# Performance work log

Measured on AMD Instinct MI355X. Metric: run time of the kernel, lower is better.

## Reference

```python
import jax, jax.numpy as jnp
import numpy as np

H = 8        # num_heads
HKV = 4      # kv_heads
WINDOW = 12  # sliding-window size (Chebyshev distance on the 2D grid)
BASE = 10000.0


def _rope_tables(N, head_dim, base=BASE):
    """2D axial RoPE for a square grid: first half of head_dim -> H pos, second -> W pos."""
    side = int(round(N ** 0.5))
    assert side * side == N
    dq = head_dim // 4
    inv = 1.0 / (base ** (np.arange(dq, dtype=np.float32) / dq))
    gh, gw = np.meshgrid(np.arange(side, dtype=np.float32), np.arange(side, dtype=np.float32), indexing='ij')
    th = np.outer(gh.ravel(), inv)   # [N, dq]
    tw = np.outer(gw.ravel(), inv)   # [N, dq]
    theta = np.concatenate([th, tw], axis=1)        # [N, head_dim//2]
    theta = np.concatenate([theta, theta], axis=1)  # [N, head_dim]
    return jnp.asarray(np.cos(theta)), jnp.asarray(np.sin(theta))


def _window_mask(N, window):
    """Additive mask: -inf where Chebyshev distance on the sqrt(N) x sqrt(N) grid > window."""
    side = int(round(N ** 0.5))
    idx = np.arange(side)
    gh, gw = np.meshgrid(idx, idx, indexing='ij')
    coords = np.stack([gh.ravel(), gw.ravel()], axis=1)            # [N, 2]
    dist = np.abs(coords[:, None, :] - coords[None, :, :]).max(-1)  # [N, N]
    return jnp.asarray(np.where(dist > window, -np.inf, 0.0).astype(np.float32))


def _rotate_half(x):
    x1, x2 = jnp.split(x, 2, axis=-1)
    return jnp.concatenate([-x2, x1], axis=-1)


def _apply_rope(x, cos, sin):
    # x: [B,H,N,d]; cos/sin: [N,d] broadcast over batch/heads
    return x * cos + _rotate_half(x) * sin


def _l2norm(x, eps=1e-12):
    return x / jnp.sqrt(jnp.sum(x * x, axis=-1, keepdims=True) + eps)


def setup_inputs() -> dict:
    key = jax.random.key(0)
    ks = jax.random.split(key, 7)
    B, N, C = 4, 2304, 512
    x = jax.random.normal(ks[0], (B, N, C), dtype=jnp.float32)
    Wq = jax.random.normal(ks[1], (C, 2 * C), dtype=jnp.float32) * 0.02
    Wk = jax.random.normal(ks[2], (C, 2 * C * HKV // H), dtype=jnp.float32) * 0.02
    Wv1 = jax.random.normal(ks[3], (C, C * HKV // H), dtype=jnp.float32) * 0.02
    Wv2 = jax.random.normal(ks[4], (C, C * HKV // H), dtype=jnp.float32) * 0.02
    lambda_p = jnp.full((H, 1, 1), -2.0, dtype=jnp.float32)
    Wp = jax.random.normal(ks[5], (C, C), dtype=jnp.float32) * 0.02
    bp = jnp.zeros((C,), dtype=jnp.float32)
    return {"x": x, "Wq": Wq, "Wk": Wk, "Wv1": Wv1, "Wv2": Wv2,
            "lambda_p": lambda_p, "Wp": Wp, "bp": bp}


def reference(x, Wq, Wk, Wv1, Wv2, lambda_p, Wp, bp):
    B, N, C = x.shape
    d = C // H
    scale = d ** -0.5
    cos, sin = _rope_tables(N, d)
    mask = _window_mask(N, WINDOW)  # [N,N] additive

    def to_heads(t, h):  # [B,N,h*d] -> [B,h,N,d]
        return t.reshape(B, N, h, -1).transpose(0, 2, 1, 3)

    q = x @ Wq                                  # [B,N,2C]
    q1, q2 = jnp.split(q, 2, axis=-1)
    q1, q2 = to_heads(q1, H), to_heads(q2, H)   # [B,H,N,d]
    k = x @ Wk                                  # [B,N,2*C*HKV/H]
    k1, k2 = jnp.split(k, 2, axis=-1)
    k1, k2 = to_heads(k1, HKV), to_heads(k2, HKV)  # [B,HKV,N,d]
    v1 = to_heads(x @ Wv1, HKV)
    v2 = to_heads(x @ Wv2, HKV)

    # QK-norm (L2) then RoPE
    q1, q2, k1, k2 = (_l2norm(t) for t in (q1, q2, k1, k2))
    q1 = _apply_rope(q1, cos, sin)
    q2 = _apply_rope(q2, cos, sin)
    k1 = _apply_rope(k1, cos, sin)
    k2 = _apply_rope(k2, cos, sin)

    # GQA: repeat KV heads to match query heads
    rep = H // HKV
    k1, k2 = jnp.repeat(k1, rep, axis=1), jnp.repeat(k2, rep, axis=1)
    v1, v2 = jnp.repeat(v1, rep, axis=1), jnp.repeat(v2, rep, axis=1)

    attn1 = jax.nn.softmax(jnp.einsum('bhnd,bhmd->bhnm', q1, k1) * scale + mask, axis=-1)
    attn2 = jax.nn.softmax(jnp.einsum('bhnd,bhmd->bhnm', q2, k2) * scale + mask, axis=-1)
    lam = jax.nn.sigmoid(lambda_p)[None]  # [1,H,1,1]
    out = jnp.einsum('bhnm,bhmd->bhnd', attn1, v1) - lam * jnp.einsum('bhnm,bhmd->bhnd', attn2, v2)
    out = out.transpose(0, 2, 1, 3).reshape(B, N, C)
    return out @ Wp + bp
```

## Files before the change

### kernel.cpp

```cpp
#include <hip/hip_runtime.h>
#include <stdint.h>

typedef unsigned short u16;
typedef __attribute__((ext_vector_type(8))) short bf16x8;
typedef __attribute__((ext_vector_type(4))) float f32x4;

#define LOG2E 1.4426950408889634f

__device__ __forceinline__ float bf2f(u16 u) {
    union { uint32_t i; float f; } v; v.i = ((uint32_t)u) << 16; return v.f;
}
__device__ __forceinline__ u16 f2bf(float f) {
    union { float f; uint32_t i; } v; v.f = f;
    uint32_t i = v.i;
    return (u16)((i + 0x7FFF + ((i >> 16) & 1)) >> 16);
}
__device__ __forceinline__ uint32_t cvt_pk_bf16(float a, float b) {
    uint32_t r;
    asm("v_cvt_pk_bf16_f32 %0, %1, %2" : "=v"(r) : "v"(a), "v"(b));
    return r;
}
__device__ __forceinline__ int imin(int a, int b) { return a < b ? a : b; }
__device__ __forceinline__ int imax(int a, int b) { return a > b ? a : b; }

__device__ __forceinline__ void gl_lds16(const void* g, void* l) {
    __builtin_amdgcn_global_load_lds(
        (const __attribute__((address_space(1))) uint32_t*)g,
        (__attribute__((address_space(3))) uint32_t*)l, 16, 0, 0);
}

__device__ __forceinline__ float exp2_poly(float t) {
    const float c1 = 0.6931471805599453f;
    const float c2 = 0.2402265069591007f;
    const float c3 = 0.05550410866482158f;
    float p = fmaf(c3, t, c2);
    p = fmaf(p, t, c1);
    return fmaf(p, t, 1.0f);
}

union U8 { bf16x8 v; uint32_t u[4]; };

__global__ void k_prep(const float* __restrict__ x,
                       const float* __restrict__ Wq, const float* __restrict__ Wk,
                       const float* __restrict__ Wv1, const float* __restrict__ Wv2,
                       const float* __restrict__ Wp,
                       float* __restrict__ tab, u16* __restrict__ xb,
                       u16* __restrict__ WCT, u16* __restrict__ WPT) {
    __shared__ u16 tile[64][65];
    int bid = blockIdx.x;
    if (bid < 288) {
        int t = bid * 256 + threadIdx.x;
        if (t >= 2304 * 32) return;
        int n = t >> 5, j = t & 31;
        int gh = n / 48, gw = n % 48;
        float f = (float)(j & 15);
        float coord = (j < 16) ? (float)gh : (float)gw;
        float inv = exp2f(-f * (13.287712379549449f / 16.0f));
        float th = coord * inv;
        tab[t * 2 + 0] = cosf(th);
        tab[t * 2 + 1] = sinf(th);
    } else if (bid < 4896) {
        int t = (bid - 288) * 256 + threadIdx.x;
        if (t >= 9216 * 512 / 4) return;
        float4 v = ((const float4*)x)[t];
        ushort4 o;
        o.x = f2bf(v.x); o.y = f2bf(v.y); o.z = f2bf(v.z); o.w = f2bf(v.w);
        ((ushort4*)xb)[t] = o;
    } else {
        int jb = bid - 4896;
        int n0 = (jb % 40) * 64;
        int k0 = (jb / 40) * 64;
        int c = threadIdx.x & 63;
        int rr = threadIdx.x >> 6;
        const float* src; int stride; int roff; u16* dst; int nb;
        if (n0 < 1024)      { src = Wq;  stride = 1024; roff = 0;    dst = WCT; nb = n0; }
        else if (n0 < 1536) { src = Wk;  stride = 512;  roff = 1024; dst = WCT; nb = n0; }
        else if (n0 < 1792) { src = Wv1; stride = 256;  roff = 1536; dst = WCT; nb = n0; }
        else if (n0 < 2048) { src = Wv2; stride = 256;  roff = 1792; dst = WCT; nb = n0; }
        else                { src = Wp;  stride = 512;  roff = 2048; dst = WPT; nb = n0 - 2048; }
        int scol = n0 + c - roff;
#pragma unroll
        for (int i = 0; i < 16; ++i) {
            int k = rr * 16 + i;
            tile[c][k] = f2bf(src[(size_t)(k0 + k) * stride + scol]);
        }
        __syncthreads();
        int kk = threadIdx.x & 63;
        int c4 = threadIdx.x >> 6;
#pragma unroll
        for (int i = 0; i < 16; ++i) {
            int nl = c4 * 16 + i;
            dst[(size_t)(nb + nl) * 512 + k0 + kk] = tile[nl][kk];
        }
    }
}

__global__ __launch_bounds__(256) void k_gemm_qkv(
    const u16* __restrict__ A, const u16* __restrict__ BT,
    const float* __restrict__ tab,
    u16* __restrict__ Q1, u16* __restrict__ Q2,
    u16* __restrict__ KF1, u16* __restrict__ KF2,
    u16* __restrict__ VF1, u16* __restrict__ VF2) {
    __shared__ u16 Asw[128 * 64];
    __shared__ u16 Bsw[128 * 64];
    const int K = 512;
    int id = blockIdx.x + 16 * blockIdx.y;
    int l = (id & 7) * 144 + (id >> 3);
    int n0 = (l & 15) * 128;
    int m0 = (l >> 4) * 128;
    int tid = threadIdx.x;
    int lane = tid & 63, w = tid >> 6;
    int wm = w >> 1, wn = w & 1;
    int li = lane & 15, g = lane >> 4;
    f32x4 zero4 = {0.f, 0.f, 0.f, 0.f};
    f32x4 acc[4][4];
#pragma unroll
    for (int mi = 0; mi < 4; ++mi)
#pragma unroll
        for (int ni = 0; ni < 4; ++ni) acc[mi][ni] = zero4;

    for (int k0 = 0; k0 < K; k0 += 64) {
        __syncthreads();
#pragma unroll
        for (int p = 0; p < 4; ++p) {
            int cidx = p * 256 + tid;
            int r = cidx >> 3, j = cidx & 7;
            int jj = j ^ (r & 7);
            gl_lds16(A  + (size_t)(m0 + r) * K + k0 + jj * 8, (char*)Asw + cidx * 16);
            gl_lds16(BT + (size_t)(n0 + r) * K + k0 + jj * 8, (char*)Bsw + cidx * 16);
        }
        __syncthreads();
#pragma unroll
        for (int ks = 0; ks < 2; ++ks) {
            bf16x8 af[4], bfr[4];
#pragma unroll
            for (int mi = 0; mi < 4; ++mi) {
                int r = wm * 64 + mi * 16 + li;
                int kc = ks * 4 + g;
                af[mi] = *(const bf16x8*)((const char*)Asw + r * 128 + ((kc ^ (r & 7)) * 16));
            }
#pragma unroll
            for (int ni = 0; ni < 4; ++ni) {
                int r = wn * 64 + ni * 16 + li;
                int kc = ks * 4 + g;
                bfr[ni] = *(const bf16x8*)((const char*)Bsw + r * 128 + ((kc ^ (r & 7)) * 16));
            }
#pragma unroll
            for (int mi = 0; mi < 4; ++mi)
#pragma unroll
                for (int ni = 0; ni < 4; ++ni)
                    acc[mi][ni] = __builtin_amdgcn_mfma_f32_16x16x32_bf16(af[mi], bfr[ni], acc[mi][ni], 0, 0, 0);
        }
    }

    int colbase = n0 + wn * 64;
    int b = m0 / 2304;
    int nbase = (m0 % 2304) + wm * 64;

    if (colbase < 1536) {
        u16* out; int isK; size_t hb;
        if (colbase < 1024) {
            out = (colbase < 512) ? Q1 : Q2;
            int h = (colbase >> 6) & 7;
            hb = (size_t)(b * 8 + h) * 2304;
            isK = 0;
        } else {
            out = (colbase < 1280) ? KF1 : KF2;
            int hkv = ((colbase - 1024) >> 6) & 3;
            hb = (size_t)(b * 4 + hkv) * 48;
            isK = 1;
        }
#pragma unroll
        for (int mi = 0; mi < 4; ++mi) {
            float rsq[4];
#pragma unroll
            for (int r = 0; r < 4; ++r) {
                float ss = 0.f;
#pragma unroll
                for (int ni = 0; ni < 4; ++ni) ss += acc[mi][ni][r] * acc[mi][ni][r];
                ss += __shfl_xor(ss, 1, 64);
                ss += __shfl_xor(ss, 2, 64);
                ss += __shfl_xor(ss, 4, 64);
                ss += __shfl_xor(ss, 8, 64);
                rsq[r] = 1.0f / sqrtf(ss + 1e-12f);
            }
#pragma unroll
            for (int r = 0; r < 4; ++r) {
                int n = nbase + mi * 16 + g * 4 + r;
                float2 cs0 = *(const float2*)(tab + ((size_t)n * 32 + li) * 2);
                float2 cs1 = *(const float2*)(tab + ((size_t)n * 32 + 16 + li) * 2);
                float y[4];
#pragma unroll
                for (int ni = 0; ni < 4; ++ni) {
                    float c = (ni & 1) ? cs1.x : cs0.x;
                    float s = (ni & 1) ? cs1.y : cs0.y;
                    float p = acc[mi][ni ^ 2][r];
                    float t = (ni < 2) ? (acc[mi][ni][r] * c - p * s)
                                       : (acc[mi][ni][r] * c + p * s);
                    y[ni] = t * rsq[r];
                }
                if (!isK) {
                    size_t obase = (hb + n) * 64;
#pragma unroll
                    for (int ni = 0; ni < 4; ++ni)
                        out[obase + ni * 16 + li] = f2bf(y[ni]);
                } else {
                    int kh = n / 48, r48 = n % 48;
                    int kt = r48 >> 4, lq = r48 & 15;
                    size_t base = (hb + kh) * 3072;
#pragma unroll
                    for (int ni = 0; ni < 4; ++ni) {
                        int sC = ni >> 1;
                        int gg = ((ni & 1) << 1) + (li >> 3);
                        int e = li & 7;
                        out[base + (size_t)(((kt * 2 + sC) * 64 + gg * 16 + lq) * 8 + e)] = f2bf(y[ni]);
                    }
                }
            }
        }
    } else {
        u16* out = (colbase < 1792) ? VF1 : VF2;
        int hkv = ((colbase - 1536) >> 6) & 3;
        size_t hb = (size_t)(b * 4 + hkv) * 48;
#pragma unroll
        for (int mi = 0; mi < 4; ++mi) {
            int n4 = nbase + mi * 16 + g * 4;
            int kh = n4 / 48, r48 = n4 % 48;
            int grp = r48 >> 2;
            int kt = grp >> 2, gp = grp & 3;
            size_t base = (hb + kh) * 3072;
#pragma unroll
            for (int ni = 0; ni < 4; ++ni) {
                uint2 val;
                val.x = cvt_pk_bf16(acc[mi][ni][0], acc[mi][ni][1]);
                val.y = cvt_pk_bf16(acc[mi][ni][2], acc[mi][ni][3]);
                *(uint2*)(out + base + (size_t)(((ni * 3 + kt) * 64 + gp * 16 + li) * 4)) = val;
            }
        }
    }
}

__global__ __launch_bounds__(256) void k_gemm_o64(
    const u16* __restrict__ A, const u16* __restrict__ BT,
    float* __restrict__ Cout, const float* __restrict__ bias) {
    __shared__ u16 Asw[64 * 64];
    __shared__ u16 Bsw[64 * 64];
    const int K = 512;
    const int N = 512;
    int id = blockIdx.x + 8 * blockIdx.y;
    int l = (id & 7) * 144 + (id >> 3);
    int n0 = (l & 7) * 64;
    int m0 = (l >> 3) * 64;
    int tid = threadIdx.x;
    int lane = tid & 63, w = tid >> 6;
    int wm = w >> 1, wn = w & 1;
    int li = lane & 15, g = lane >> 4;
    f32x4 zero4 = {0.f, 0.f, 0.f, 0.f};
    f32x4 acc[2][2];
#pragma unroll
    for (int mi = 0; mi < 2; ++mi)
#pragma unroll
        for (int ni = 0; ni < 2; ++ni) acc[mi][ni] = zero4;

    for (int k0 = 0; k0 < K; k0 += 64) {
        __syncthreads();
#pragma unroll
        for (int p = 0; p < 2; ++p) {
            int ci = p * 256 + tid;
            int r = ci >> 3, j = ci & 7;
            int jj = j ^ (r & 7);
            gl_lds16(A  + (size_t)(m0 + r) * K + k0 + jj * 8, (char*)Asw + ci * 16);
            gl_lds16(BT + (size_t)(n0 + r) * K + k0 + jj * 8, (char*)Bsw + ci * 16);
        }
        __syncthreads();
#pragma unroll
        for (int ks = 0; ks < 2; ++ks) {
            bf16x8 af[2], bfr[2];
#pragma unroll
            for (int mi = 0; mi < 2; ++mi) {
                int r = wm * 32 + mi * 16 + li;
                int kc = ks * 4 + g;
                af[mi] = *(const bf16x8*)((const char*)Asw + r * 128 + ((kc ^ (r & 7)) * 16));
            }
#pragma unroll
            for (int ni = 0; ni < 2; ++ni) {
                int r = wn * 32 + ni * 16 + li;
                int kc = ks * 4 + g;
                bfr[ni] = *(const bf16x8*)((const char*)Bsw + r * 128 + ((kc ^ (r & 7)) * 16));
            }
#pragma unroll
            for (int mi = 0; mi < 2; ++mi)
#pragma unroll
                for (int ni = 0; ni < 2; ++ni)
                    acc[mi][ni] = __builtin_amdgcn_mfma_f32_16x16x32_bf16(af[mi], bfr[ni], acc[mi][ni], 0, 0, 0);
        }
    }
#pragma unroll
    for (int mi = 0; mi < 2; ++mi)
#pragma unroll
        for (int ni = 0; ni < 2; ++ni) {
#pragma unroll
            for (int r = 0; r < 4; ++r) {
                int row = m0 + wm * 32 + mi * 16 + g * 4 + r;
                int col = n0 + wn * 32 + ni * 16 + li;
                Cout[(size_t)row * N + col] = acc[mi][ni][r] + bias[col];
            }
        }
}

template <int A, int NTT>
__device__ __forceinline__ void load_k(const u16* __restrict__ kb, bf16x8 (&kf)[NTT][2], int lane) {
#pragma unroll
    for (int t = 0; t < NTT; ++t)
#pragma unroll
        for (int s = 0; s < 2; ++s)
            kf[t][s] = *(const bf16x8*)(kb + ((A + t) * 2 + s) * 512 + lane * 8);
}

template <int A, int NTT>
__device__ __forceinline__ void attn_compute(
    const bf16x8 (&kf)[NTT][2], const u16* __restrict__ vb,
    const bf16x8 (&qf)[2][2], const float (&bmul)[3][4],
    f32x4 (&Oa)[2][4], float (&sum)[2], int lane) {
    const float SC = 0.125f * LOG2E;
    uint2 ch[4][NTT];
#pragma unroll
    for (int dt = 0; dt < 4; ++dt)
#pragma unroll
        for (int t = 0; t < NTT; ++t)
            ch[dt][t] = *(const uint2*)(vb + ((dt * 3 + A + t) * 64 + lane) * 4);
    __builtin_amdgcn_s_setprio(1);
    U8 pa0[2], pa1[2];
#pragma unroll
    for (int h = 0; h < 2; ++h) {
        f32x4 S[NTT];
#pragma unroll
        for (int t = 0; t < NTT; ++t) {
            f32x4 z = {0.f, 0.f, 0.f, 0.f};
            z = __builtin_amdgcn_mfma_f32_16x16x32_bf16(kf[t][0], qf[h][0], z, 0, 0, 0);
            S[t] = __builtin_amdgcn_mfma_f32_16x16x32_bf16(kf[t][1], qf[h][1], z, 0, 0, 0);
        }
        uint32_t pk[NTT][2];
#pragma unroll
        for (int t = 0; t < NTT; ++t)
#pragma unroll
            for (int rp = 0; rp < 2; ++rp) {
                float p0 = exp2_poly(S[t][2 * rp]     * SC) * bmul[A + t][2 * rp];
                float p1 = exp2_poly(S[t][2 * rp + 1] * SC) * bmul[A + t][2 * rp + 1];
                sum[h] += p0 + p1;
                pk[t][rp] = cvt_pk_bf16(p0, p1);
            }
        pa0[h].u[0] = pk[0][0]; pa0[h].u[1] = pk[0][1];
        pa0[h].u[2] = pk[1][0]; pa0[h].u[3] = pk[1][1];
        if (NTT == 3) { pa1[h].u[0] = pk[2][0]; pa1[h].u[1] = pk[2][1]; pa1[h].u[2] = 0; pa1[h].u[3] = 0; }
    }
#pragma unroll
    for (int dt = 0; dt < 4; ++dt) {
        union { bf16x8 v; uint2 q[2]; } vf0, vf1;
        vf0.q[0] = ch[dt][0]; vf0.q[1] = ch[dt][1];
        if (NTT == 3) { vf1.q[0] = ch[dt][2]; vf1.q[1] = ch[dt][2]; }
#pragma unroll
        for (int h = 0; h < 2; ++h) {
            Oa[h][dt] = __builtin_amdgcn_mfma_f32_16x16x32_bf16(pa0[h].v, vf0.v, Oa[h][dt], 0, 0, 0);
            if (NTT == 3)
                Oa[h][dt] = __builtin_amdgcn_mfma_f32_16x16x32_bf16(pa1[h].v, vf1.v, Oa[h][dt], 0, 0, 0);
        }
    }
    __builtin_amdgcn_s_setprio(0);
}

template <int A, int NTT>
__device__ __forceinline__ void run_range(
    const u16* __restrict__ kp, const u16* __restrict__ vp, int n,
    const bf16x8 (&qf)[2][2], const float (&bmul)[3][4],
    f32x4 (&Oa)[2][4], float (&sum)[2], int lane) {
    bf16x8 kA[NTT][2], kB[NTT][2];
    load_k<A, NTT>(kp, kA, lane);
    int i = 0;
    for (; i + 2 <= n; i += 2) {
        load_k<A, NTT>(kp + 3072, kB, lane);
        attn_compute<A, NTT>(kA, vp, qf, bmul, Oa, sum, lane);
        load_k<A, NTT>(kp + ((i + 3 <= n) ? 6144 : 3072), kA, lane);
        attn_compute<A, NTT>(kB, vp + 3072, qf, bmul, Oa, sum, lane);
        kp += 6144; vp += 6144;
    }
    if (i < n) attn_compute<A, NTT>(kA, vp, qf, bmul, Oa, sum, lane);
}

__global__ __launch_bounds__(128) void k_attention(
    const u16* __restrict__ Q1, const u16* __restrict__ Q2,
    const u16* __restrict__ KF1, const u16* __restrict__ KF2,
    const u16* __restrict__ VF1, const u16* __restrict__ VF2,
    const float* __restrict__ lambda_p, u16* __restrict__ AOUT) {
    __shared__ float obuf[2][16][64];
    int tid = threadIdx.x;
    int lane = tid & 63, beta = tid >> 6;
    int li = lane & 15, g = lane >> 4;
    int hw = blockIdx.x;
    int l = (hw & 7) * 288 + (hw >> 3);
    int mu = l % 3, j = (l / 3) % 48, kvb = l / 144;
    int m2 = j >> 1;
    int qh = (j & 1) ? (23 - m2) : (24 + m2);
    int hkv = kvb & 3, b = kvb >> 2;

    const u16* Qb = beta ? Q2 : Q1;

    bf16x8 qf[2][2];
#pragma unroll
    for (int h2 = 0; h2 < 2; ++h2)
#pragma unroll
        for (int s = 0; s < 2; ++s)
            qf[h2][s] = *(const bf16x8*)(Qb + ((size_t)(b * 8 + hkv * 2 + h2) * 2304
                            + qh * 48 + mu * 16 + li) * 64 + s * 32 + g * 8);

    float bmul[3][4];
    int qw = mu * 16 + li;
#pragma unroll
    for (int t = 0; t < 3; ++t)
#pragma unroll
        for (int r = 0; r < 4; ++r) {
            int kw = t * 16 + 4 * g + r;
            int dw = qw - kw; if (dw < 0) dw = -dw;
            bmul[t][r] = (dw <= 12) ? 1.0f : 0.0f;
        }

    f32x4 zero4 = {0.f, 0.f, 0.f, 0.f};
    f32x4 Oa[2][4];
#pragma unroll
    for (int h = 0; h < 2; ++h)
#pragma unroll
        for (int dt = 0; dt < 4; ++dt) Oa[h][dt] = zero4;
    float sum[2] = {0.f, 0.f};

    int kh0 = imax(0, qh - 12), kh1 = imin(47, qh + 12);
    int niter = kh1 - kh0 + 1;
    const u16* kp = (beta ? KF2 : KF1) + ((size_t)kvb * 48 + kh0) * 3072;
    const u16* vp = (beta ? VF2 : VF1) + ((size_t)kvb * 48 + kh0) * 3072;

    if (mu == 1)      run_range<0, 3>(kp, vp, niter, qf, bmul, Oa, sum, lane);
    else if (mu == 0) run_range<0, 2>(kp, vp, niter, qf, bmul, Oa, sum, lane);
    else              run_range<1, 2>(kp, vp, niter, qf, bmul, Oa, sum, lane);

    float inv[2][4];
#pragma unroll
    for (int h = 0; h < 2; ++h) {
        float s = sum[h];
        s += __shfl_xor(s, 16, 64);
        s += __shfl_xor(s, 32, 64);
#pragma unroll
        for (int r = 0; r < 4; ++r)
            inv[h][r] = 1.0f / __shfl(s, 4 * g + r, 64);
    }

    if (beta == 1) {
#pragma unroll
        for (int h = 0; h < 2; ++h)
#pragma unroll
            for (int dt = 0; dt < 4; ++dt)
#pragma unroll
                for (int r = 0; r < 4; ++r)
                    obuf[h][4 * g + r][dt * 16 + li] = Oa[h][dt][r] * inv[h][r];
    }
    __syncthreads();
    if (beta == 0) {
#pragma unroll
        for (int h = 0; h < 2; ++h) {
            float lam = 1.0f / (1.0f + expf(-lambda_p[hkv * 2 + h]));
#pragma unroll
            for (int dt = 0; dt < 4; ++dt)
#pragma unroll
                for (int r = 0; r < 4; ++r) {
                    float o1 = Oa[h][dt][r] * inv[h][r];
                    float o2 = obuf[h][4 * g + r][dt * 16 + li];
                    int n = qh * 48 + mu * 16 + 4 * g + r;
                    int colc = (hkv * 2 + h) * 64 + dt * 16 + li;
                    AOUT[((size_t)(b * 2304 + n)) * 512 + colc] = f2bf(o1 - lam * o2);
                }
        }
    }
}

extern "C" void kernel_launch(void* const* d_in, const int* in_sizes, int n_in,
                              void* d_out, int out_size, void* d_ws, size_t ws_size,
                              hipStream_t stream) {
    const float* x        = (const float*)d_in[0];
    const float* Wq       = (const float*)d_in[1];
    const float* Wk       = (const float*)d_in[2];
    const float* Wv1      = (const float*)d_in[3];
    const float* Wv2      = (const float*)d_in[4];
    const float* lambda_p = (const float*)d_in[5];
    const float* Wp       = (const float*)d_in[6];
    const float* bp       = (const float*)d_in[7];

    char* ws = (char*)d_ws;
    size_t off = 0;
    auto alloc = [&](size_t bytes) { char* p = ws + off; off += (bytes + 255) & ~(size_t)255; return p; };
    float* rope = (float*)alloc((size_t)2304 * 32 * 2 * 4);
    u16* XB     = (u16*)alloc((size_t)9216 * 512 * 2);
    u16* WCT    = (u16*)alloc((size_t)2048 * 512 * 2);
    u16* WPT    = (u16*)alloc((size_t)512 * 512 * 2);
    u16* Q1     = (u16*)alloc((size_t)4 * 8 * 2304 * 64 * 2);
    u16* Q2     = (u16*)alloc((size_t)4 * 8 * 2304 * 64 * 2);
    u16* KF1    = (u16*)alloc((size_t)16 * 48 * 3072 * 2);
    u16* KF2    = (u16*)alloc((size_t)16 * 48 * 3072 * 2);
    u16* VF1    = (u16*)alloc((size_t)16 * 48 * 3072 * 2);
    u16* VF2    = (u16*)alloc((size_t)16 * 48 * 3072 * 2);
    u16* AOUT   = (u16*)alloc((size_t)9216 * 512 * 2);

    k_prep<<<5216, 256, 0, stream>>>(x, Wq, Wk, Wv1, Wv2, Wp, rope, XB, WCT, WPT);
    k_gemm_qkv<<<dim3(16, 72), 256, 0, stream>>>(XB, WCT, rope, Q1, Q2, KF1, KF2, VF1, VF2);
    k_attention<<<2304, 128, 0, stream>>>(Q1, Q2, KF1, KF2, VF1, VF2, lambda_p, AOUT);
    k_gemm_o64<<<dim3(8, 144), 256, 0, stream>>>(AOUT, WPT, (float*)d_out, bp);
}
```

Measured before the change: 124.0 us.

## Prefetch V alongside K, fold softmax scale into Q, shorten exp2 polynomial

The softmax scale (0.125*log2e) is folded into the Q normalization in the projection epilogue, which removes a multiply per score in the attention inner loop. The cubic exp2 polynomial becomes a quadratic with adjusted coefficients, cutting one FMA per element at some cost in accuracy. For the two-tile (mu 0 and 2) cases, V fragments are now double-buffered and prefetched one step ahead together with K, hiding V load latency at the cost of more registers. Note that exp2 of an unreduced argument via a low-order polynomial is only accurate for small arguments; it relies on L2-normed q,k keeping scores small.

```diff
diff --git a/kernel.cpp b/kernel.cpp
--- a/kernel.cpp
+++ b/kernel.cpp
@@ -6,6 +6,7 @@
 typedef __attribute__((ext_vector_type(4))) float f32x4;
 
 #define LOG2E 1.4426950408889634f
+#define QSCALE (0.125f * LOG2E)
 
 __device__ __forceinline__ float bf2f(u16 u) {
     union { uint32_t i; float f; } v; v.i = ((uint32_t)u) << 16; return v.f;
@@ -29,13 +30,10 @@
         (__attribute__((address_space(3))) uint32_t*)l, 16, 0, 0);
 }
 
-__device__ __forceinline__ float exp2_poly(float t) {
-    const float c1 = 0.6931471805599453f;
-    const float c2 = 0.2402265069591007f;
-    const float c3 = 0.05550410866482158f;
-    float p = fmaf(c3, t, c2);
-    p = fmaf(p, t, c1);
-    return fmaf(p, t, 1.0f);
+__device__ __forceinline__ float exp2q(float t) {
+    const float a = 0.6946474805f;
+    const float b = 0.2402265069f;
+    return fmaf(fmaf(b, t, a), t, 1.0f);
 }
 
 union U8 { bf16x8 v; uint32_t u[4]; };
@@ -170,6 +168,7 @@
             hb = (size_t)(b * 4 + hkv) * 48;
             isK = 1;
         }
+        float qs = isK ? 1.0f : QSCALE;
 #pragma unroll
         for (int mi = 0; mi < 4; ++mi) {
             float rsq[4];
@@ -182,7 +181,7 @@
                 ss += __shfl_xor(ss, 2, 64);
                 ss += __shfl_xor(ss, 4, 64);
                 ss += __shfl_xor(ss, 8, 64);
-                rsq[r] = 1.0f / sqrtf(ss + 1e-12f);
+                rsq[r] = qs / sqrtf(ss + 1e-12f);
             }
 #pragma unroll
             for (int r = 0; r < 4; ++r) {
@@ -318,17 +317,19 @@
 }
 
 template <int A, int NTT>
-__device__ __forceinline__ void attn_compute(
-    const bf16x8 (&kf)[NTT][2], const u16* __restrict__ vb,
-    const bf16x8 (&qf)[2][2], const float (&bmul)[3][4],
-    f32x4 (&Oa)[2][4], float (&sum)[2], int lane) {
-    const float SC = 0.125f * LOG2E;
-    uint2 ch[4][NTT];
+__device__ __forceinline__ void load_v(const u16* __restrict__ vb, uint2 (&ch)[4][NTT], int lane) {
 #pragma unroll
     for (int dt = 0; dt < 4; ++dt)
 #pragma unroll
         for (int t = 0; t < NTT; ++t)
             ch[dt][t] = *(const uint2*)(vb + ((dt * 3 + A + t) * 64 + lane) * 4);
+}
+
+template <int A, int NTT>
+__device__ __forceinline__ void attn_core(
+    const bf16x8 (&kf)[NTT][2], const uint2 (&ch)[4][NTT],
+    const bf16x8 (&qf)[2][2], const float (&bmul)[3][4],
+    f32x4 (&Oa)[2][4], float (&sum)[2]) {
     __builtin_amdgcn_s_setprio(1);
     U8 pa0[2], pa1[2];
 #pragma unroll
@@ -345,8 +346,8 @@
         for (int t = 0; t < NTT; ++t)
 #pragma unroll
             for (int rp = 0; rp < 2; ++rp) {
-                float p0 = exp2_poly(S[t][2 * rp]     * SC) * bmul[A + t][2 * rp];
-                float p1 = exp2_poly(S[t][2 * rp + 1] * SC) * bmul[A + t][2 * rp + 1];
+                float p0 = exp2q(S[t][2 * rp])     * bmul[A + t][2 * rp];
+                float p1 = exp2q(S[t][2 * rp + 1]) * bmul[A + t][2 * rp + 1];
                 sum[h] += p0 + p1;
                 pk[t][rp] = cvt_pk_bf16(p0, p1);
             }
@@ -367,6 +368,16 @@
         }
     }
     __builtin_amdgcn_s_setprio(0);
+}
+
+template <int A, int NTT>
+__device__ __forceinline__ void attn_step_local(
+    const bf16x8 (&kf)[NTT][2], const u16* __restrict__ vb,
+    const bf16x8 (&qf)[2][2], const float (&bmul)[3][4],
+    f32x4 (&Oa)[2][4], float (&sum)[2], int lane) {
+    uint2 ch[4][NTT];
+    load_v<A, NTT>(vb, ch, lane);
+    attn_core<A, NTT>(kf, ch, qf, bmul, Oa, sum);
 }
 
 template <int A, int NTT>
@@ -379,12 +390,35 @@
     int i = 0;
     for (; i + 2 <= n; i += 2) {
         load_k<A, NTT>(kp + 3072, kB, lane);
-        attn_compute<A, NTT>(kA, vp, qf, bmul, Oa, sum, lane);
+        attn_step_local<A, NTT>(kA, vp, qf, bmul, Oa, sum, lane);
         load_k<A, NTT>(kp + ((i + 3 <= n) ? 6144 : 3072), kA, lane);
-        attn_compute<A, NTT>(kB, vp + 3072, qf, bmul, Oa, sum, lane);
+        attn_step_local<A, NTT>(kB, vp + 3072, qf, bmul, Oa, sum, lane);
         kp += 6144; vp += 6144;
     }
-    if (i < n) attn_compute<A, NTT>(kA, vp, qf, bmul, Oa, sum, lane);
+    if (i < n) attn_step_local<A, NTT>(kA, vp, qf, bmul, Oa, sum, lane);
+}
+
+template <int A>
+__device__ __forceinline__ void run_range_pf(
+    const u16* __restrict__ kp, const u16* __restrict__ vp, int n,
+    const bf16x8 (&qf)[2][2], const float (&bmul)[3][4],
+    f32x4 (&Oa)[2][4], float (&sum)[2], int lane) {
+    bf16x8 kA[2][2], kB[2][2];
+    uint2 vA[4][2], vB[4][2];
+    load_k<A, 2>(kp, kA, lane);
+    load_v<A, 2>(vp, vA, lane);
+    int i = 0;
+    for (; i + 2 <= n; i += 2) {
+        load_k<A, 2>(kp + 3072, kB, lane);
+        load_v<A, 2>(vp + 3072, vB, lane);
+        attn_core<A, 2>(kA, vA, qf, bmul, Oa, sum);
+        int adv = (i + 3 <= n) ? 6144 : 3072;
+        load_k<A, 2>(kp + adv, kA, lane);
+        load_v<A, 2>(vp + adv, vA, lane);
+        attn_core<A, 2>(kB, vB, qf, bmul, Oa, sum);
+        kp += 6144; vp += 6144;
+    }
+    if (i < n) attn_core<A, 2>(kA, vA, qf, bmul, Oa, sum);
 }
 
 __global__ __launch_bounds__(128) void k_attention(
@@ -438,8 +472,8 @@
     const u16* vp = (beta ? VF2 : VF1) + ((size_t)kvb * 48 + kh0) * 3072;
 
     if (mu == 1)      run_range<0, 3>(kp, vp, niter, qf, bmul, Oa, sum, lane);
-    else if (mu == 0) run_range<0, 2>(kp, vp, niter, qf, bmul, Oa, sum, lane);
-    else              run_range<1, 2>(kp, vp, niter, qf, bmul, Oa, sum, lane);
+    else if (mu == 0) run_range_pf<0>(kp, vp, niter, qf, bmul, Oa, sum, lane);
+    else              run_range_pf<1>(kp, vp, niter, qf, bmul, Oa, sum, lane);
 
     float inv[2][4];
 #pragma unroll
```

After: 120.3 us, median of 3. -2.9%, faster.
